# Optimization experiments

Measured on AMD Instinct MI355X. Metric: run time of the kernel, lower is better.

Reference implementation:

```python
import jax, jax.numpy as jnp
import numpy as np

B, C, L, H, P, NF = 32, 512, 336, 1024, 192, 4  # batch, enc_in, seq_len, nflow_dim, pred_len, nflow_layers


def setup_inputs() -> dict:
    key = jax.random.key(0)
    ks = jax.random.split(key, 18)
    s = 0.02  # small init so exp(0.5*sigma) stays tame
    f32 = jnp.float32
    return {
        "x_enc": jax.random.normal(ks[0], (B, C, L), f32),
        "eps": jax.random.normal(ks[1], (B, C, P), f32),
        # GRU params (torch gate order r,z,n)
        "gru_wih": jax.random.normal(ks[2], (3 * H, C), f32) * s,
        "gru_whh": jax.random.normal(ks[3], (3 * H, H), f32) * s,
        "gru_bih": jax.random.normal(ks[4], (3 * H,), f32) * s,
        "gru_bhh": jax.random.normal(ks[5], (3 * H,), f32) * s,
        # enc_fix: Linear(1, enc_in)
        "encfix_w": jax.random.normal(ks[6], (C, 1), f32) * s,
        "encfix_b": jax.random.normal(ks[7], (C,), f32) * s,
        # distribution_enc_mu / presigma: Linear(d_ff, pred_len)
        "encmu_w": jax.random.normal(ks[8], (P, H), f32) * s,
        "encmu_b": jax.random.normal(ks[9], (P,), f32) * s,
        "encps_w": jax.random.normal(ks[10], (P, H), f32) * s,
        "encps_b": jax.random.normal(ks[11], (P,), f32) * s,
        # flow layers (stacked): Conv1d(C,C,2), Linear(H+P,P) x2
        "conv_w": jax.random.normal(ks[12], (NF, C, C, 2), f32) * s,
        "conv_b": jax.random.normal(ks[13], (NF, C), f32) * s,
        "mu_w": jax.random.normal(ks[14], (NF, P, H + P), f32) * s,
        "mu_b": jax.random.normal(ks[15], (NF, P), f32) * s,
        "sg_w": jax.random.normal(ks[16], (NF, P, H + P), f32) * s,
        "sg_b": jax.random.normal(ks[17], (NF, P), f32) * s,
    }


def reference(x_enc, eps, gru_wih, gru_whh, gru_bih, gru_bhh,
              encfix_w, encfix_b, encmu_w, encmu_b, encps_w, encps_b,
              conv_w, conv_b, mu_w, mu_b, sg_w, sg_b):
    h_dim = gru_whh.shape[1]
    pred_len = encmu_w.shape[0]
    x = jnp.transpose(x_enc, (0, 2, 1))            # (B, L, C)
    xw = x @ gru_wih.T + gru_bih                   # (B, L, 3H) input projections, precomputed

    def step(h, g):
        gh = h @ gru_whh.T + gru_bhh
        ir, iz, in_ = jnp.split(g, 3, axis=-1)
        hr, hz, hn = jnp.split(gh, 3, axis=-1)
        r = jax.nn.sigmoid(ir + hr)
        z = jax.nn.sigmoid(iz + hz)
        n = jnp.tanh(in_ + r * hn)
        return (1.0 - z) * n + z * h, None

    h0 = jnp.zeros((x.shape[0], h_dim), x.dtype)
    hT, _ = jax.lax.scan(step, h0, jnp.swapaxes(xw, 0, 1))  # (B, H) final hidden

    # enc_fix: Linear(1, enc_in) applied on last axis of (B, H, 1)
    enc = hT[:, :, None] * encfix_w[:, 0] + encfix_b        # (B, H, C)
    enc = jnp.transpose(enc, (0, 2, 1))                      # (B, C, H)

    enc_mu = enc @ encmu_w.T + encmu_b                       # (B, C, P)
    enc_sigma = jax.nn.softplus(enc @ encps_w.T + encps_b)   # (B, C, P)
    sample = enc_mu + jnp.exp(0.5 * enc_sigma) * eps         # (B, C, P)
    h = jnp.concatenate([enc, sample], axis=2)               # (B, C, H+P)

    for l in range(conv_w.shape[0]):
        w = conv_w[l]                                        # (C, C, 2)
        # Conv1d kernel size 2, valid padding, then ReLU
        hc = (jnp.einsum('bit,oi->bot', h[:, :, :-1], w[:, :, 0])
              + jnp.einsum('bit,oi->bot', h[:, :, 1:], w[:, :, 1])
              + conv_b[l][:, None])
        hc = jax.nn.relu(hc)
        hc = jnp.concatenate([hc[:, :, :1], hc], axis=2)     # re-pad to (B, C, H+P)
        mu = hc @ mu_w[l].T + mu_b[l]                        # (B, C, P)
        sg = hc @ sg_w[l].T + sg_b[l]                        # (B, C, P)
        sample = mu + jnp.exp(0.5 * sg) * sample * 0.1
        h = h + 0.1 * jnp.concatenate([hc[:, :, :hc.shape[2] - pred_len], sample], axis=2)

    return jnp.transpose(sample, (0, 2, 1))                  # (B, P, C)
```

## Files before the change

### kernel.cpp

```cpp
#include <hip/hip_runtime.h>

using u16 = unsigned short;
using u32 = unsigned int;
using u64 = unsigned long long;
using f32x4 = __attribute__((ext_vector_type(4))) float;
using s16x8 = __attribute__((ext_vector_type(8))) short;
using u32x4 = __attribute__((ext_vector_type(4))) unsigned int;

__device__ __forceinline__ u16 f2b(float f) {
  union { float f; u32 u; } v; v.f = f;
  u32 r = v.u + 0x7fffu + ((v.u >> 16) & 1u);
  return (u16)(r >> 16);
}
__device__ __forceinline__ float b2f(u16 h) {
  union { u32 u; float f; } v; v.u = ((u32)h) << 16; return v.f;
}
__device__ __forceinline__ void gl_lds16(const u16* g, u16* l) {
  __builtin_amdgcn_global_load_lds(
      (const __attribute__((address_space(1))) void*)g,
      (__attribute__((address_space(3))) void*)l, 16, 0, 0);
}
__device__ __forceinline__ float fsigm(float x) {
  return 1.f / (1.f + __expf(-x));
}
__device__ __forceinline__ float ftanh(float x) {
  float ax = fabsf(x);
  float e2 = __expf(2.f * ax);
  float th = 1.f - 2.f / (e2 + 1.f);
  return copysignf(th, x);
}

__global__ void k_cast(const float* __restrict__ s, u16* __restrict__ d, int n) {
  int i = blockIdx.x * 256 + threadIdx.x;
  if (i < n) d[i] = f2b(s[i]);
}

__global__ void k_musgw(const float* __restrict__ muw, const float* __restrict__ sgw,
                        u16* __restrict__ dst, int n) {
  int i = blockIdx.x * 256 + threadIdx.x;
  if (i >= n) return;
  int l = i / (384 * 1216);
  int r = (i / 1216) % 384;
  int k = i % 1216;
  int p = r >> 1;
  const float* s = (r & 1) ? (sgw + ((long)l * 192 + p) * 1216 + k)
                           : (muw + ((long)l * 192 + p) * 1216 + k);
  dst[i] = f2b(*s);
}

__global__ void k_catb(const float* __restrict__ mub, const float* __restrict__ sgb,
                       float* __restrict__ catb) {
  int i = blockIdx.x * 256 + threadIdx.x;
  if (i >= 1536) return;
  int l = i / 384, r = i % 384;
  int p = r >> 1;
  catb[i] = (r & 1) ? sgb[l * 192 + p] : mub[l * 192 + p];
}

__global__ void k_convw(const float* __restrict__ cw, u16* __restrict__ Aw, int n) {
  int i = blockIdx.x * 256 + threadIdx.x;
  if (i >= n) return;
  int l = i >> 19;
  int r1 = i & 524287;
  int o = r1 >> 10;
  int r2 = r1 & 1023;
  int tap = r2 >> 9;
  int ii = r2 & 511;
  Aw[i] = f2b(cw[(((long)(l * 512 + o)) * 512 + ii) * 2 + tap]);
}

__global__ void k_gruw(const float* __restrict__ whh, u16* __restrict__ blob) {
  int i = blockIdx.x * 256 + threadIdx.x;
  int lane = i & 63;
  int c = (i >> 6) & 15;
  int g = (i >> 10) % 3;
  int wwv = i / 3072;
  int wv = wwv & 3, wg = wwv >> 2;
  int jbw = wv & 1, kw = wv >> 1;
  int j = wg * 32 + jbw * 16 + (lane & 15);
  int k = kw * 512 + c * 32 + (lane >> 4) * 8;
  const float* src = whh + ((long)(g * 1024 + j)) * 1024 + k;
  u16* dst = blob + (long)i * 8;
#pragma unroll
  for (int v = 0; v < 8; ++v) dst[v] = f2b(src[v]);
}

__global__ __launch_bounds__(256) void k_txe(const float* __restrict__ x, u16* __restrict__ xT) {
  __shared__ float tile[32][33];
  int l0 = blockIdx.x * 32, c0 = blockIdx.y * 32, b = blockIdx.z;
  int tid = threadIdx.x;
  for (int q = 0; q < 4; ++q) {
    int idx = tid + q * 256;
    int r = idx >> 5, cc = idx & 31;
    int l = l0 + cc;
    tile[r][cc] = (l < 336) ? x[((long)b * 512 + c0 + r) * 336 + l] : 0.f;
  }
  __syncthreads();
  for (int q = 0; q < 4; ++q) {
    int idx = tid + q * 256;
    int r = idx >> 5, cc = idx & 31;
    int l = l0 + r;
    if (l < 336) xT[((long)b * 336 + l) * 512 + c0 + cc] = f2b(tile[cc][r]);
  }
}

__global__ __launch_bounds__(256) void k_hbt(const float* __restrict__ hbuf, u16* __restrict__ hbT) {
  __shared__ float tile[32][65];
  int t0 = blockIdx.x * 64, c0 = blockIdx.y * 32, b = blockIdx.z;
  int tid = threadIdx.x;
#pragma unroll
  for (int q = 0; q < 2; ++q) {
    int idx = tid + q * 256;
    int r = idx >> 4, col = (idx & 15) * 4;
    *(float4*)&tile[r][col] =
        *(const float4*)&hbuf[((long)b * 512 + c0 + r) * 1216 + t0 + col];
  }
  __syncthreads();
#pragma unroll
  for (int q = 0; q < 2; ++q) {
    int idx = tid + q * 256;
    int t = idx >> 3, cg = (idx & 7) * 4;
    ushort4 o;
    o.x = f2b(tile[cg + 0][t]);
    o.y = f2b(tile[cg + 1][t]);
    o.z = f2b(tile[cg + 2][t]);
    o.w = f2b(tile[cg + 3][t]);
    *(ushort4*)&hbT[((long)b * 1216 + t0 + t) * 512 + c0 + cg] = o;
  }
}

__global__ __launch_bounds__(256) void k_out(const float* __restrict__ smp, float* __restrict__ out) {
  __shared__ float tile[32][33];
  int p0 = blockIdx.x * 32, c0 = blockIdx.y * 32, b = blockIdx.z;
  int tid = threadIdx.x;
  for (int q = 0; q < 4; ++q) {
    int idx = tid + q * 256;
    int r = idx >> 5, cc = idx & 31;
    tile[r][cc] = smp[((long)b * 512 + c0 + r) * 192 + p0 + cc];
  }
  __syncthreads();
  for (int q = 0; q < 4; ++q) {
    int idx = tid + q * 256;
    int r = idx >> 5, cc = idx & 31;
    out[((long)b * 192 + p0 + r) * 512 + c0 + cc] = tile[cc][r];
  }
}

template<int MODE, int TPZ = 0, int NX = 1>
__global__ __launch_bounds__(256, 2)
void gemm_bt(const u16* __restrict__ A, const u16* __restrict__ Bt,
             void* __restrict__ Cv, const float* __restrict__ bias,
             int M, int N, int K, int lda, int ldb, int ldc,
             long sA, long sB, long sC,
             int arowmax, int browmax, int NT,
             float* __restrict__ hbufp, long sH,
             float* __restrict__ sampleP, long sS)
{
  __shared__ u16 As[128 * 64];
  __shared__ u16 Bs[128 * 64];
  const int tid = threadIdx.x;
  const int lane = tid & 63;
  const int wv = tid >> 6;
  int bx, by, bz;
  if (TPZ > 0) {
    int bid = (int)blockIdx.x;
    int xcd = bid & 7, idx = bid >> 3;
    int zhi = idx / TPZ, r = idx - zhi * TPZ;
    bz = zhi * 8 + xcd;
    by = r / NX;
    bx = r - by * NX;
  } else {
    bx = (int)blockIdx.x; by = (int)blockIdx.y; bz = (int)blockIdx.z;
  }
  const int z = bz;
  const u16* Ab = A + (long)z * sA;
  const u16* Bb = Bt + (long)z * sB;
  const int m0 = by * 128, n0 = bx * 128;
  const int wm = (wv >> 1) * 64, wn = (wv & 1) * 64;

  f32x4 acc[4][4] = {};

  for (int kt = 0; kt < K; kt += 64) {
#pragma unroll
    for (int s = 0; s < 4; ++s) {
      int row = (wv * 4 + s) * 8 + (lane >> 3);
      int ck = (lane & 7) ^ (row & 7);
      int ra = m0 + row; if (ra > arowmax) ra = arowmax;
      gl_lds16(Ab + (long)ra * lda + (kt + ck * 8), As + (wv * 4 + s) * 512);
      int rb = n0 + row; if (rb > browmax) rb = browmax;
      gl_lds16(Bb + (long)rb * ldb + (kt + ck * 8), Bs + (wv * 4 + s) * 512);
    }
    __syncthreads();
#pragma unroll
    for (int kk = 0; kk < 64; kk += 32) {
      s16x8 af[4], bfr[4];
#pragma unroll
      for (int i = 0; i < 4; ++i) {
        int rowa = wm + i * 16 + (lane & 15);
        int offa = (rowa * 128 + (kk + 8 * (lane >> 4)) * 2) ^ ((rowa & 7) << 4);
        af[i] = *(const s16x8*)((const char*)As + offa);
        int rowb = wn + i * 16 + (lane & 15);
        int offb = (rowb * 128 + (kk + 8 * (lane >> 4)) * 2) ^ ((rowb & 7) << 4);
        bfr[i] = *(const s16x8*)((const char*)Bs + offb);
      }
#pragma unroll
      for (int i = 0; i < 4; ++i)
#pragma unroll
        for (int j = 0; j < 4; ++j)
          acc[i][j] = __builtin_amdgcn_mfma_f32_16x16x32_bf16(af[i], bfr[j], acc[i][j], 0, 0, 0);
    }
    __syncthreads();
  }

  u16* Cb16 = (u16*)Cv;
#pragma unroll
  for (int i = 0; i < 4; ++i) {
#pragma unroll
    for (int j = 0; j < 4; ++j) {
      const int mb = m0 + wm + i * 16 + 4 * (lane >> 4);
      const int n = n0 + wn + j * 16 + (lane & 15);
      if (n >= NT) continue;
      f32x4 v = acc[i][j];
      if (MODE == 0) {
        float bn = bias[n];
        u16* Cp = Cb16;
#pragma unroll
        for (int r = 0; r < 4; ++r)
          Cp[(long)(mb + r) * ldc + n] = f2b(v[r] + bn);
      } else if (MODE == 4) {
        float bn = bias[n];
        u16* Cp = Cb16;
#pragma unroll
        for (int r = 0; r < 4; ++r) {
          int m = mb + r;
          int bb = m / 336;
          int tt = m - bb * 336;
          Cp[(long)(tt * 32 + bb) * ldc + n] = f2b(v[r] + bn);
        }
      } else if (MODE == 2) {
        u16* Cp = Cb16 + (long)z * sC;
        float* hb = hbufp + (long)z * sH;
#pragma unroll
        for (int r = 0; r < 4; ++r) {
          int m = mb + r;
          float x = v[r] + bias[m];
          x = fmaxf(x, 0.0f);
          u16 hx = f2b(x);
          Cp[(long)m * ldc + (n + 1)] = hx;
          if (n + 1 < 1024) hb[(long)m * 1216 + (n + 1)] += 0.1f * x;
          if (n == 0) { Cp[(long)m * ldc] = hx; hb[(long)m * 1216] += 0.1f * x; }
        }
      } else {
        float bn = bias[n];
        float* hb = hbufp + (long)z * sH;
        float* smp = sampleP + (long)z * sS;
        const int p = n >> 1;
#pragma unroll
        for (int r = 0; r < 4; ++r) {
          float val = v[r] + bn;
          float other = __shfl_xor(val, 1);
          if ((lane & 1) == 0) {
            int m = mb + r;
            long si = (long)m * 192 + p;
            float snew = val + __expf(0.5f * other) * smp[si] * 0.1f;
            smp[si] = snew;
            hb[(long)m * 1216 + 1024 + p] += 0.1f * snew;
          }
        }
      }
    }
  }
}

__global__ __launch_bounds__(256, 1)
void k_gru(const u16* __restrict__ xw, const u16* __restrict__ wblob,
           const float* __restrict__ bhh, u64* __restrict__ hfA, u64* __restrict__ hfB,
           float* __restrict__ hTt, float* __restrict__ hTn, u32* __restrict__ flags)
{
  __shared__ float part[6][32][32];
  const int tid = threadIdx.x;
  const int lane = tid & 63;
  const int wv = tid >> 6;
  const int q = (int)(blockIdx.x >> 5);
  const int tw = (int)(blockIdx.x & 31);
  const int jbw = wv & 1, kw = wv >> 1;
  u32* __restrict__ myflags = flags + q * 1024;

  s16x8 bfr[3][16];
  {
    const u16* wp = wblob + (long)(tw * 4 + wv) * 24576 + lane * 8;
#pragma unroll
    for (int g = 0; g < 3; ++g)
#pragma unroll
      for (int c = 0; c < 16; ++c)
        bfr[g][c] = *(const s16x8*)(wp + (g * 16 + c) * 512);
  }

  const int bq16 = tid & 15, jg = (tid >> 4) & 7;
  const int j0 = tw * 32 + jg * 4;
  const int bb = q * 16 + bq16;
  float b3[3][4];
#pragma unroll
  for (int g = 0; g < 3; ++g)
#pragma unroll
    for (int jj = 0; jj < 4; ++jj) b3[g][jj] = bhh[g * 1024 + j0 + jj];
  ushort4 hold = make_ushort4(0, 0, 0, 0);

  const long hoff64 = (long)(tw * 2 + q) * 128 + ((long)(jg >> 1) * 16 + bq16) * 2;
  const int myflag = tw * 32;

  for (int t = 0; t < 336; ++t) {
    const u64* __restrict__ hr = (t & 1) ? hfB : hfA;
    u64* __restrict__ hw = (t & 1) ? hfA : hfB;

    ushort4 xr = {}, xz = {}, xn = {};
    if (tid < 128) {
      const u16* xp = xw + ((long)t * 32 + bb) * 3072 + j0;
      xr = *(const ushort4*)(xp);
      xz = *(const ushort4*)(xp + 1024);
      xn = *(const ushort4*)(xp + 2048);
    }

    if (t > 0) {
      if (wv == 0) {
        const int fi = (lane & 31) * 32;
        int spins = 0;
        while (true) {
          u32 v = __hip_atomic_load(&myflags[fi], __ATOMIC_RELAXED, __HIP_MEMORY_SCOPE_AGENT);
          if (__ballot(v >= (u32)t) == ~0ull) break;
          __builtin_amdgcn_s_sleep(1);
          if (++spins > (1 << 22)) break;
        }
      }
    }
    __syncthreads();
    __builtin_amdgcn_sched_barrier(0);

    u32x4 md[16];
#pragma unroll
    for (int c = 0; c < 16; ++c) {
      const int cg = kw * 16 + c;
      u64 a0 = (u64)(const void*)(hr + ((long)(cg * 2 + q) * 64 + lane) * 2);
      asm volatile("global_load_dwordx4 %0, %1, off sc1" : "=v"(md[c]) : "v"(a0) : "memory");
    }
    asm volatile("s_waitcnt vmcnt(0)" ::: "memory");
    __builtin_amdgcn_sched_barrier(0);

    f32x4 acc[3] = {};
#pragma unroll
    for (int c = 0; c < 16; ++c) {
      union { u32x4 d; s16x8 v; } au;
      au.d = md[c];
#pragma unroll
      for (int g = 0; g < 3; ++g)
        acc[g] = __builtin_amdgcn_mfma_f32_16x16x32_bf16(au.v, bfr[g][c], acc[g], 0, 0, 0);
    }
    {
      const int jl = jbw * 16 + (lane & 15);
      const int swz = ((jl & 1) << 4) | ((jl & 6) << 1);
      const int s4 = (lane >> 4) * 4;
#pragma unroll
      for (int g = 0; g < 3; ++g)
        *(f32x4*)&part[kw * 3 + g][jl][(16 * q + s4) ^ swz] = acc[g];
    }
    __syncthreads();

    if (tid < 128) {
      float hnew[4];
#pragma unroll
      for (int jj = 0; jj < 4; ++jj) {
        const int jl = jg * 4 + jj;
        const int swz = ((jl & 1) << 4) | ((jl & 6) << 1);
        const int slot = (16 * q + bq16) ^ swz;
        float s0 = part[0][jl][slot] + part[3][jl][slot] + b3[0][jj];
        float s1 = part[1][jl][slot] + part[4][jl][slot] + b3[1][jj];
        float s2 = part[2][jl][slot] + part[5][jl][slot] + b3[2][jj];
        float xrv = b2f(((const u16*)&xr)[jj]);
        float xzv = b2f(((const u16*)&xz)[jj]);
        float xnv = b2f(((const u16*)&xn)[jj]);
        float rg = fsigm(xrv + s0);
        float zg = fsigm(xzv + s1);
        float ng = ftanh(xnv + rg * s2);
        float holdv = b2f(((const u16*)&hold)[jj]);
        hnew[jj] = (1.f - zg) * ng + zg * holdv;
      }
      ((u16*)&hold)[0] = f2b(hnew[0]);
      ((u16*)&hold)[1] = f2b(hnew[1]);
      ((u16*)&hold)[2] = f2b(hnew[2]);
      ((u16*)&hold)[3] = f2b(hnew[3]);

      {
        union { ushort4 s; u32 d[2]; } hq; hq.s = hold;
        u32 p0 = (u32)__shfl_xor((int)hq.d[0], 16);
        u32 p1 = (u32)__shfl_xor((int)hq.d[1], 16);
        if ((lane & 16) == 0) {
          union { u32 d[4]; u32x4 v; } st;
          st.d[0] = hq.d[0]; st.d[1] = hq.d[1]; st.d[2] = p0; st.d[3] = p1;
          u64 ad = (u64)(void*)(hw + hoff64);
          asm volatile("global_store_dwordx4 %0, %1, off sc1" :: "v"(ad), "v"(st.v) : "memory");
        }
      }
      if (t == 335) {
#pragma unroll
        for (int jj = 0; jj < 4; ++jj) hTt[(j0 + jj) * 32 + bb] = hnew[jj];
        *(float4*)(hTn + bb * 1024 + j0) = make_float4(hnew[0], hnew[1], hnew[2], hnew[3]);
      }
    }
    asm volatile("s_waitcnt vmcnt(0)" ::: "memory");
    __syncthreads();
    if (tid == 0)
      __hip_atomic_store(&myflags[myflag], (u32)(t + 1), __ATOMIC_RELAXED, __HIP_MEMORY_SCOPE_AGENT);
  }
}

__global__ __launch_bounds__(256) void k_encsmall(
    const float* __restrict__ hTt, const float* __restrict__ emw, const float* __restrict__ epw,
    float* __restrict__ Am, float* __restrict__ Asg, float* __restrict__ Sm, float* __restrict__ Ssg)
{
  int q = blockIdx.x * 256 + threadIdx.x;
  int p = q >> 3, bg = q & 7;
  float am[4] = {0.f, 0.f, 0.f, 0.f}, as[4] = {0.f, 0.f, 0.f, 0.f};
  float sm = 0.f, ss = 0.f;
  const float* wmp = emw + (long)p * 1024;
  const float* wsp = epw + (long)p * 1024;
  for (int k = 0; k < 1024; ++k) {
    float a = wmp[k], b = wsp[k];
    f32x4 hv = *(const f32x4*)(hTt + k * 32 + bg * 4);
#pragma unroll
    for (int i = 0; i < 4; ++i) { am[i] += a * hv[i]; as[i] += b * hv[i]; }
    sm += a; ss += b;
  }
#pragma unroll
  for (int i = 0; i < 4; ++i) {
    Am[(bg * 4 + i) * 192 + p] = am[i];
    Asg[(bg * 4 + i) * 192 + p] = as[i];
  }
  if (bg == 0) { Sm[p] = sm; Ssg[p] = ss; }
}

__global__ __launch_bounds__(256) void k_build(
    const float* __restrict__ hTn, const float* __restrict__ fw, const float* __restrict__ fb,
    const float* __restrict__ Am, const float* __restrict__ Asg,
    const float* __restrict__ Sm, const float* __restrict__ Ssg,
    const float* __restrict__ emub, const float* __restrict__ epsb,
    const float* __restrict__ eps, float* __restrict__ hbuf, float* __restrict__ sample)
{
  int c = blockIdx.x, b = blockIdx.y, tid = threadIdx.x;
  float fwc = fw[c], fbc = fb[c];
  long hb0 = ((long)b * 512 + c) * 1216;
  const float* hrow = hTn + b * 1024;
  for (int q = 0; q < 4; ++q) {
    int tt = tid + q * 256;
    hbuf[hb0 + tt] = hrow[tt] * fwc + fbc;
  }
  if (tid < 192) {
    int p = tid;
    float mu_e = fwc * Am[b * 192 + p] + fbc * Sm[p] + emub[p];
    float pse = fwc * Asg[b * 192 + p] + fbc * Ssg[p] + epsb[p];
    float sgv = (pse > 15.f) ? pse : log1pf(__expf(pse));
    long si = ((long)b * 512 + c) * 192 + p;
    float smp = mu_e + __expf(0.5f * sgv) * eps[si];
    sample[si] = smp;
    hbuf[hb0 + 1024 + p] = smp;
  }
}

extern "C" void kernel_launch(void* const* d_in, const int* in_sizes, int n_in,
                              void* d_out, int out_size, void* d_ws, size_t ws_size,
                              hipStream_t stream)
{
  const float* x_enc = (const float*)d_in[0];
  const float* eps   = (const float*)d_in[1];
  const float* wih   = (const float*)d_in[2];
  const float* whh   = (const float*)d_in[3];
  const float* bih   = (const float*)d_in[4];
  const float* bhh   = (const float*)d_in[5];
  const float* fw    = (const float*)d_in[6];
  const float* fb    = (const float*)d_in[7];
  const float* emw   = (const float*)d_in[8];
  const float* emub  = (const float*)d_in[9];
  const float* epw   = (const float*)d_in[10];
  const float* epsb  = (const float*)d_in[11];
  const float* cw    = (const float*)d_in[12];
  const float* cb    = (const float*)d_in[13];
  const float* muw   = (const float*)d_in[14];
  const float* mub   = (const float*)d_in[15];
  const float* sgw   = (const float*)d_in[16];
  const float* sgwb  = (const float*)d_in[17];
  float* out = (float*)d_out;

  char* w = (char*)d_ws;
  auto alloc = [&](size_t bytes) { char* p = w; w += (bytes + 255) & ~(size_t)255; return p; };
  u16* Aw       = (u16*)alloc(4ull * 512 * 1024 * 2);
  u16* musgw16  = (u16*)alloc(4ull * 384 * 1216 * 2);
  u16* wih16    = (u16*)alloc(3072ull * 512 * 2);
  u64* hfA      = (u64*)alloc(65536);
  u64* hfB      = (u64*)alloc(65536);
  u32* flags    = (u32*)alloc(8192);
  float* catb   = (float*)alloc(1536 * 4);
  float* hTt    = (float*)alloc(131072);
  float* hTn    = (float*)alloc(131072);
  float* Am     = (float*)alloc(32 * 192 * 4);
  float* Asg    = (float*)alloc(32 * 192 * 4);
  float* Sm     = (float*)alloc(1024);
  float* Ssg    = (float*)alloc(1024);
  float* smp    = (float*)alloc(32ull * 512 * 192 * 4);
  u16* hcB      = (u16*)alloc(32ull * 512 * 1216 * 2);
  char* un1     = alloc(32ull * 512 * 1216 * 4);
  u16* xw       = (u16*)un1;
  float* hbuf   = (float*)un1;
  char* un2     = alloc(32ull * 1216 * 512 * 2);
  u16* xT       = (u16*)un2;
  u16* hbT      = (u16*)un2;
  u16* wblob    = hcB;

  if ((size_t)(w - (char*)d_ws) > ws_size) return;

  hipMemsetAsync(hfA, 0, 65536, stream);
  hipMemsetAsync(hfB, 0, 65536, stream);
  hipMemsetAsync(flags, 0, 8192, stream);

  k_cast<<<dim3((3072 * 512 + 255) / 256), 256, 0, stream>>>(wih, wih16, 3072 * 512);
  k_musgw<<<dim3((4 * 384 * 1216 + 255) / 256), 256, 0, stream>>>(muw, sgw, musgw16, 4 * 384 * 1216);
  k_catb<<<dim3(6), 256, 0, stream>>>(mub, sgwb, catb);
  k_convw<<<dim3((4 * 512 * 1024 + 255) / 256), 256, 0, stream>>>(cw, Aw, 4 * 512 * 1024);
  k_gruw<<<dim3(1536), 256, 0, stream>>>(whh, wblob);
  k_txe<<<dim3(11, 16, 32), 256, 0, stream>>>(x_enc, xT);

  gemm_bt<4><<<dim3(24, 84, 1), 256, 0, stream>>>(xT, wih16, xw, bih,
      10752, 3072, 512, 512, 512, 3072, 0, 0, 0, 10751, 3071, 3072,
      nullptr, 0, nullptr, 0);

  k_gru<<<dim3(64), 256, 0, stream>>>(xw, wblob, bhh, hfA, hfB, hTt, hTn, flags);

  k_encsmall<<<dim3(6), 256, 0, stream>>>(hTt, emw, epw, Am, Asg, Sm, Ssg);
  k_build<<<dim3(512, 32), 256, 0, stream>>>(hTn, fw, fb, Am, Asg, Sm, Ssg, emub, epsb, eps, hbuf, smp);

  for (int l = 0; l < 4; ++l) {
    k_hbt<<<dim3(19, 16, 32), 256, 0, stream>>>(hbuf, hbT);
    gemm_bt<2, 40, 10><<<dim3(1280), 256, 0, stream>>>(Aw + (long)l * 512 * 1024, hbT, hcB, cb + l * 512,
        512, 1215, 1024, 1024, 512, 1216, 0, 1216 * 512, 512 * 1216, 511, 1214, 1215,
        hbuf, 512 * 1216, nullptr, 0);
    gemm_bt<5, 12, 3><<<dim3(384), 256, 0, stream>>>(hcB, musgw16 + (long)l * 384 * 1216, nullptr, catb + l * 384,
        512, 384, 1216, 1216, 1216, 384, 512 * 1216, 0, 0, 511, 383, 384,
        hbuf, 512 * 1216, smp, 512 * 192);
  }

  k_out<<<dim3(6, 16, 32), 256, 0, stream>>>(smp, out);
}
```

Measured before the change: 2.063 ms.

## Overlap GRU input-projection GEMM with the recurrent scan inside one launch

Folds the x@Wih input-projection GEMM into the GRU kernel as extra blocks (2016 beyond the 64 recurrent blocks). Each GEMM block signals completion of its 128-row tile (4 timesteps × 32 batch) through a per-tile counter. The recurrent blocks spin on that counter before reading xw for a given timestep. The input transpose now writes time-major rows so the GEMM tiles align with timesteps. The goal is to hide the GEMM behind the serial recurrence and drop one launch. It relies on the 64 persistent GRU blocks being scheduled alongside the GEMM blocks, and GEMM blocks may compete for CUs with the latency-critical scan.

```diff
diff --git a/kernel.cpp b/kernel.cpp
--- a/kernel.cpp
+++ b/kernel.cpp
@@ -100,7 +100,7 @@
     int idx = tid + q * 256;
     int r = idx >> 5, cc = idx & 31;
     int l = l0 + r;
-    if (l < 336) xT[((long)b * 336 + l) * 512 + c0 + cc] = f2b(tile[cc][r]);
+    if (l < 336) xT[((long)l * 32 + b) * 512 + c0 + cc] = f2b(tile[cc][r]);
   }
 }
 
@@ -221,23 +221,7 @@
       const int n = n0 + wn + j * 16 + (lane & 15);
       if (n >= NT) continue;
       f32x4 v = acc[i][j];
-      if (MODE == 0) {
-        float bn = bias[n];
-        u16* Cp = Cb16;
-#pragma unroll
-        for (int r = 0; r < 4; ++r)
-          Cp[(long)(mb + r) * ldc + n] = f2b(v[r] + bn);
-      } else if (MODE == 4) {
-        float bn = bias[n];
-        u16* Cp = Cb16;
-#pragma unroll
-        for (int r = 0; r < 4; ++r) {
-          int m = mb + r;
-          int bb = m / 336;
-          int tt = m - bb * 336;
-          Cp[(long)(tt * 32 + bb) * ldc + n] = f2b(v[r] + bn);
-        }
-      } else if (MODE == 2) {
+      if (MODE == 2) {
         u16* Cp = Cb16 + (long)z * sC;
         float* hb = hbufp + (long)z * sH;
 #pragma unroll
@@ -273,14 +257,76 @@
 }
 
 __global__ __launch_bounds__(256, 1)
-void k_gru(const u16* __restrict__ xw, const u16* __restrict__ wblob,
-           const float* __restrict__ bhh, u64* __restrict__ hfA, u64* __restrict__ hfB,
+void k_gru(const u16* __restrict__ xT2, const u16* __restrict__ wih16,
+           const float* __restrict__ bih, u16* __restrict__ xw, u32* __restrict__ done,
+           const u16* __restrict__ wblob, const float* __restrict__ bhh,
+           u64* __restrict__ hfA, u64* __restrict__ hfB,
            float* __restrict__ hTt, float* __restrict__ hTn, u32* __restrict__ flags)
 {
-  __shared__ float part[6][32][32];
+  __shared__ __align__(16) char smem[32768];
   const int tid = threadIdx.x;
   const int lane = tid & 63;
   const int wv = tid >> 6;
+
+  if (blockIdx.x >= 64) {
+    u16* As = (u16*)smem;
+    u16* Bs = As + 8192;
+    const int bid2 = (int)blockIdx.x - 64;
+    const int by = bid2 / 24, bx = bid2 - by * 24;
+    const int m0 = by * 128, n0 = bx * 128;
+    const int wm = (wv >> 1) * 64, wn = (wv & 1) * 64;
+    f32x4 acc[4][4] = {};
+    for (int kt = 0; kt < 512; kt += 64) {
+#pragma unroll
+      for (int s = 0; s < 4; ++s) {
+        int row = (wv * 4 + s) * 8 + (lane >> 3);
+        int ck = (lane & 7) ^ (row & 7);
+        gl_lds16(xT2 + (long)(m0 + row) * 512 + (kt + ck * 8), As + (wv * 4 + s) * 512);
+        gl_lds16(wih16 + (long)(n0 + row) * 512 + (kt + ck * 8), Bs + (wv * 4 + s) * 512);
+      }
+      __syncthreads();
+#pragma unroll
+      for (int kk = 0; kk < 64; kk += 32) {
+        s16x8 af[4], bfr[4];
+#pragma unroll
+        for (int i = 0; i < 4; ++i) {
+          int rowa = wm + i * 16 + (lane & 15);
+          int offa = (rowa * 128 + (kk + 8 * (lane >> 4)) * 2) ^ ((rowa & 7) << 4);
+          af[i] = *(const s16x8*)((const char*)As + offa);
+          int rowb = wn + i * 16 + (lane & 15);
+          int offb = (rowb * 128 + (kk + 8 * (lane >> 4)) * 2) ^ ((rowb & 7) << 4);
+          bfr[i] = *(const s16x8*)((const char*)Bs + offb);
+        }
+#pragma unroll
+        for (int i = 0; i < 4; ++i)
+#pragma unroll
+          for (int j = 0; j < 4; ++j)
+            acc[i][j] = __builtin_amdgcn_mfma_f32_16x16x32_bf16(af[i], bfr[j], acc[i][j], 0, 0, 0);
+      }
+      __syncthreads();
+    }
+#pragma unroll
+    for (int i = 0; i < 4; ++i) {
+#pragma unroll
+      for (int j = 0; j < 4; ++j) {
+        const int mb = m0 + wm + i * 16 + 4 * (lane >> 4);
+        const int n = n0 + wn + j * 16 + (lane & 15);
+        float bn = bih[n];
+#pragma unroll
+        for (int r = 0; r < 4; ++r)
+          xw[(long)(mb + r) * 3072 + n] = f2b(acc[i][j][r] + bn);
+      }
+    }
+    asm volatile("s_waitcnt vmcnt(0)" ::: "memory");
+    __syncthreads();
+    if (tid == 0) {
+      __threadfence();
+      __hip_atomic_fetch_add(&done[by], 1u, __ATOMIC_RELAXED, __HIP_MEMORY_SCOPE_AGENT);
+    }
+    return;
+  }
+
+  float (*part)[32][32] = (float(*)[32][32])smem;
   const int q = (int)(blockIdx.x >> 5);
   const int tw = (int)(blockIdx.x & 31);
   const int jbw = wv & 1, kw = wv >> 1;
@@ -312,6 +358,26 @@
   for (int t = 0; t < 336; ++t) {
     const u64* __restrict__ hr = (t & 1) ? hfB : hfA;
     u64* __restrict__ hw = (t & 1) ? hfA : hfB;
+
+    if (wv == 0) {
+      int spins = 0;
+      while (true) {
+        bool ok;
+        if (lane < 32)
+          ok = (t == 0) || (__hip_atomic_load(&myflags[lane * 32], __ATOMIC_RELAXED,
+                                              __HIP_MEMORY_SCOPE_AGENT) >= (u32)t);
+        else if (lane == 32)
+          ok = (__hip_atomic_load(&done[t >> 2], __ATOMIC_RELAXED,
+                                  __HIP_MEMORY_SCOPE_AGENT) >= 24u);
+        else
+          ok = true;
+        if (__ballot(ok) == ~0ull) break;
+        __builtin_amdgcn_s_sleep(1);
+        if (++spins > (1 << 22)) break;
+      }
+    }
+    __syncthreads();
+    __builtin_amdgcn_sched_barrier(0);
 
     ushort4 xr = {}, xz = {}, xn = {};
     if (tid < 128) {
@@ -320,21 +386,6 @@
       xz = *(const ushort4*)(xp + 1024);
       xn = *(const ushort4*)(xp + 2048);
     }
-
-    if (t > 0) {
-      if (wv == 0) {
-        const int fi = (lane & 31) * 32;
-        int spins = 0;
-        while (true) {
-          u32 v = __hip_atomic_load(&myflags[fi], __ATOMIC_RELAXED, __HIP_MEMORY_SCOPE_AGENT);
-          if (__ballot(v >= (u32)t) == ~0ull) break;
-          __builtin_amdgcn_s_sleep(1);
-          if (++spins > (1 << 22)) break;
-        }
-      }
-    }
-    __syncthreads();
-    __builtin_amdgcn_sched_barrier(0);
 
     u32x4 md[16];
 #pragma unroll
@@ -496,7 +547,7 @@
   u16* wih16    = (u16*)alloc(3072ull * 512 * 2);
   u64* hfA      = (u64*)alloc(65536);
   u64* hfB      = (u64*)alloc(65536);
-  u32* flags    = (u32*)alloc(8192);
+  u32* flags    = (u32*)alloc(12288);
   float* catb   = (float*)alloc(1536 * 4);
   float* hTt    = (float*)alloc(131072);
   float* hTn    = (float*)alloc(131072);
@@ -510,28 +561,26 @@
   u16* xw       = (u16*)un1;
   float* hbuf   = (float*)un1;
   char* un2     = alloc(32ull * 1216 * 512 * 2);
-  u16* xT       = (u16*)un2;
+  u16* xT2      = (u16*)un2;
   u16* hbT      = (u16*)un2;
   u16* wblob    = hcB;
+  u32* done     = flags + 2048;
 
   if ((size_t)(w - (char*)d_ws) > ws_size) return;
 
   hipMemsetAsync(hfA, 0, 65536, stream);
   hipMemsetAsync(hfB, 0, 65536, stream);
-  hipMemsetAsync(flags, 0, 8192, stream);
+  hipMemsetAsync(flags, 0, 12288, stream);
 
   k_cast<<<dim3((3072 * 512 + 255) / 256), 256, 0, stream>>>(wih, wih16, 3072 * 512);
   k_musgw<<<dim3((4 * 384 * 1216 + 255) / 256), 256, 0, stream>>>(muw, sgw, musgw16, 4 * 384 * 1216);
   k_catb<<<dim3(6), 256, 0, stream>>>(mub, sgwb, catb);
   k_convw<<<dim3((4 * 512 * 1024 + 255) / 256), 256, 0, stream>>>(cw, Aw, 4 * 512 * 1024);
   k_gruw<<<dim3(1536), 256, 0, stream>>>(whh, wblob);
-  k_txe<<<dim3(11, 16, 32), 256, 0, stream>>>(x_enc, xT);
-
-  gemm_bt<4><<<dim3(24, 84, 1), 256, 0, stream>>>(xT, wih16, xw, bih,
-      10752, 3072, 512, 512, 512, 3072, 0, 0, 0, 10751, 3071, 3072,
-      nullptr, 0, nullptr, 0);
-
-  k_gru<<<dim3(64), 256, 0, stream>>>(xw, wblob, bhh, hfA, hfB, hTt, hTn, flags);
+  k_txe<<<dim3(11, 16, 32), 256, 0, stream>>>(x_enc, xT2);
+
+  k_gru<<<dim3(2080), 256, 0, stream>>>(xT2, wih16, bih, xw, done,
+                                        wblob, bhh, hfA, hfB, hTt, hTn, flags);
 
   k_encsmall<<<dim3(6), 256, 0, stream>>>(hTt, emw, epw, Am, Asg, Sm, Ssg);
   k_build<<<dim3(512, 32), 256, 0, stream>>>(hTn, fw, fb, Am, Asg, Sm, Ssg, emub, epsb, eps, hbuf, smp);
```

New measurement: 2.185 ms. +6.0%, slower.
